# Optimization experiments

Measured on AMD Instinct MI355X. Metric: run time of the kernel, lower is better.

## Reference

```python
import jax, jax.numpy as jnp
import numpy as np

B, C, T, W, H = 2, 256, 16, 64, 64


def setup_inputs():
    key = jax.random.key(0)
    ks = jax.random.split(key, 6)
    C2 = C // 2
    return {
        "x": jax.random.normal(ks[0], (B, C, T, W, H), jnp.float32),
        "Wq": jax.random.normal(ks[1], (3, C2, C), jnp.float32) * 0.02,
        "bq": jnp.zeros((3, C2), jnp.float32),
        "Wk": jax.random.normal(ks[2], (3, C2, C), jnp.float32) * 0.02,
        "bk": jnp.zeros((3, C2), jnp.float32),
        "Wv": jax.random.normal(ks[3], (3, C, C), jnp.float32) * 0.02,
        "bv": jnp.zeros((3, C), jnp.float32),
        "gamma": jax.random.normal(ks[4], (3,), jnp.float32) * 0.1,
    }


def _conv1x1(t, Wm, b):
    # Conv3d with kernel_size=1 == per-voxel channel matmul
    return jnp.einsum('bcijk,oc->boijk', t, Wm) + b[None, :, None, None, None]


def _pool(t):
    # MaxPool3d(kernel=(2,1,1), stride=(2,1,1)) along dim 2 (even length)
    return jnp.maximum(t[:, :, 0::2], t[:, :, 1::2])


def _cell(x, Wq, bq, Wk, bk, Wv, bv, gamma, attn_id):
    Bb, Cc, Tt, Ww, Hh = x.shape
    if attn_id == 'T':
        out = x
    elif attn_id == 'W':
        out = jnp.swapaxes(x, 2, 3)  # [B,C,W,T,H]
    else:
        out = jnp.swapaxes(x, 2, 4)  # [B,C,H,W,T]
    A = out.shape[2]
    # NOTE: these are raw row-major reshapes, faithful to torch .view
    q = _conv1x1(out, Wq, bq).reshape(Bb, A, -1)              # [B, A, C/2*d1*d2]
    k = _pool(_conv1x1(out, Wk, bk)).reshape(Bb, -1, A // 2)  # [B, C/2*d1*d2, A/2]
    attn = jax.nn.softmax(jnp.einsum('bij,bjk->bik', q, k), axis=-1)  # [B, A, A/2]
    v = _pool(_conv1x1(out, Wv, bv)).reshape(Bb, -1, A // 2)  # [B, C*d1*d2, A/2]
    o = jnp.einsum('bxp,bap->bxa', v, attn)                   # [B, X, A]
    if attn_id == 'T':
        o = o.reshape(Bb, Cc, Ww, Hh, Tt).transpose(0, 1, 4, 2, 3)
    elif attn_id == 'W':
        o = o.reshape(Bb, Cc, Tt, Hh, Ww).transpose(0, 1, 2, 4, 3)
    else:
        o = o.reshape(Bb, Cc, Tt, Ww, Hh)
    return gamma * o + x


def reference(x, Wq, bq, Wk, bk, Wv, bv, gamma):
    out = x
    for i, aid in enumerate(('T', 'W', 'H')):
        out = _cell(out, Wq[i], bq[i], Wk[i], bk[i], Wv[i], bv[i], gamma[i], aid)
    return out
```

## Files before the change

### kernel.cpp

```cpp
#include <hip/hip_runtime.h>


constexpr int XBS = 16777216;

typedef __attribute__((ext_vector_type(8)))  short short8v;
typedef __attribute__((ext_vector_type(16))) float f32x16;

__device__ __forceinline__ unsigned rne16(float f) {
    unsigned u = __float_as_uint(f);
    return (u + 0x7FFFu + ((u >> 16) & 1u)) >> 16;
}

__global__ __launch_bounds__(64) void prep_w(
    const float* __restrict__ W, unsigned int* __restrict__ dst)
{
    const int l = threadIdx.x;
    const int ks = blockIdx.x, mf = blockIdx.y, hl = blockIdx.z;
    const float* src = W + (mf * 32 + (l & 31)) * 256 + ks * 16 + ((l >> 5) << 3);
    unsigned pk[4];
    #pragma unroll
    for (int e = 0; e < 4; ++e) {
        float f0 = src[2 * e], f1 = src[2 * e + 1];
        unsigned b0, b1;
        if (hl == 0) {
            b0 = __float_as_uint(f0) >> 16;
            b1 = __float_as_uint(f1) >> 16;
        } else {
            unsigned h0 = __float_as_uint(f0) & 0xFFFF0000u;
            unsigned h1 = __float_as_uint(f1) & 0xFFFF0000u;
            b0 = rne16(f0 - __uint_as_float(h0));
            b1 = rne16(f1 - __uint_as_float(h1));
        }
        pk[e] = b0 | (b1 << 16);
    }
    size_t off = ((size_t)(mf * 16 + ks) * 2 + hl) * 256 + l * 4;
    *(uint4*)&dst[off] = make_uint4(pk[0], pk[1], pk[2], pk[3]);
}

template<int CELL>
__global__ __launch_bounds__(256) void xsplit_kernel(
    const float* __restrict__ src, unsigned int* __restrict__ xTp)
{
    __shared__ float T[64][66];
    const int tid = threadIdx.x;
    const int b = blockIdx.z, cb = blockIdx.y, nb = blockIdx.x;
    const int runbase = (CELL == 0) ? nb * 64
                                    : ((nb & 15) * 4096 + ((nb >> 4) << 6));
    const float* sp = src + (size_t)b * XBS + (size_t)(cb * 64) * 65536 + runbase;
    #pragma unroll
    for (int i = 0; i < 4; ++i) {
        int id = tid + i * 256;
        int cl = id >> 4, rc = (id & 15) * 4;
        const float4 v = *(const float4*)&sp[(size_t)cl * 65536 + rc];
        *(float2*)&T[cl][rc]     = make_float2(v.x, v.y);
        *(float2*)&T[cl][rc + 2] = make_float2(v.z, v.w);
    }
    __syncthreads();
    unsigned int* dst = xTp + (size_t)b * (65536u * 256u);
    #pragma unroll
    for (int ps = 0; ps < 4; ++ps) {
        int r = ps * 16 + (tid >> 4);
        int c0 = (tid & 15) * 4;
        unsigned pk[4];
        #pragma unroll
        for (int e = 0; e < 4; ++e) {
            float f = T[c0 + e][r];
            unsigned hi = __float_as_uint(f) & 0xFFFF0000u;
            pk[e] = hi | rne16(f - __uint_as_float(hi));
        }
        int n_row = (CELL == 2) ? (r * 1024 + nb) : (nb * 64 + r);
        *(uint4*)&dst[(size_t)n_row * 256 + cb * 64 + c0] =
            make_uint4(pk[0], pk[1], pk[2], pk[3]);
    }
}

template<bool POOL, int LGS>
__global__ __launch_bounds__(256, 2) void mconv(
    const unsigned int* __restrict__ xTp, const unsigned int* __restrict__ wf,
    const float* __restrict__ bias, float* __restrict__ out, int obs)
{
    constexpr int NS = POOL ? 32768 : 65536;
    constexpr int MF = POOL ? 2 : 4;
    constexpr int NV = POOL ? 2 : 1;

    __shared__ __align__(16) unsigned short Bh[128 * 64];
    __shared__ __align__(16) unsigned short Bl[128 * 64];

    const int tid = threadIdx.x;
    const int lane = tid & 63, wv = tid >> 6;
    const int b = blockIdx.z, gy = blockIdx.y, nb = blockIdx.x;
    const unsigned int* xb = xTp + (size_t)b * (65536u * 256u);

    f32x16 acc[MF][NV];
    #pragma unroll
    for (int m = 0; m < MF; ++m)
        #pragma unroll
        for (int v = 0; v < NV; ++v)
            #pragma unroll
            for (int r = 0; r < 16; ++r) acc[m][v][r] = 0.f;

    for (int ko = 0; ko < 4; ++ko) {
        const int c0u = ko * 64;
        #pragma unroll
        for (int i = 0; i < 8; ++i) {
            int id = tid + i * 256;
            int row = id >> 4, q4 = id & 15;
            int n_src;
            if (!POOL) n_src = nb * 128 + row;
            else {
                int v = row >> 6, m = nb * 64 + (row & 63);
                int p = m >> LGS, s = m & ((1 << LGS) - 1);
                n_src = ((2 * p + v) << LGS) + s;
            }
            const uint4 g = *(const uint4*)&xb[(size_t)n_src * 256 + c0u + q4 * 4];
            unsigned h01 = (g.x >> 16)     | (g.y & 0xFFFF0000u);
            unsigned h23 = (g.z >> 16)     | (g.w & 0xFFFF0000u);
            unsigned l01 = (g.x & 0xFFFFu) | (g.y << 16);
            unsigned l23 = (g.z & 0xFFFFu) | (g.w << 16);
            int byt = row * 128 + (((q4 >> 1) ^ (row & 7)) << 4) + ((q4 & 1) << 3);
            *(uint2*)((char*)Bh + byt) = make_uint2(h01, h23);
            *(uint2*)((char*)Bl + byt) = make_uint2(l01, l23);
        }
        __syncthreads();
        #pragma unroll
        for (int ks = 0; ks < 4; ++ks) {
            short8v ah[MF], al[MF];
            #pragma unroll
            for (int m = 0; m < MF; ++m) {
                int mfG = gy * 4 + (POOL ? ((wv >> 1) * 2 + m) : m);
                const unsigned int* ap =
                    wf + (size_t)((mfG * 16 + ko * 4 + ks) * 2) * 256 + lane * 4;
                ah[m] = *(const short8v*)ap;
                al[m] = *(const short8v*)(ap + 256);
            }
            #pragma unroll
            for (int v = 0; v < NV; ++v) {
                int row = POOL ? (v * 64 + (wv & 1) * 32 + (lane & 31))
                               : (wv * 32 + (lane & 31));
                int byt = row * 128 + (((ks * 2 + (lane >> 5)) ^ (row & 7)) << 4);
                short8v bh = *(const short8v*)((char*)Bh + byt);
                short8v bl = *(const short8v*)((char*)Bl + byt);
                #pragma unroll
                for (int m = 0; m < MF; ++m) {
                    acc[m][v] = __builtin_amdgcn_mfma_f32_32x32x16_bf16(ah[m], bh, acc[m][v], 0, 0, 0);
                    acc[m][v] = __builtin_amdgcn_mfma_f32_32x32x16_bf16(ah[m], bl, acc[m][v], 0, 0, 0);
                    acc[m][v] = __builtin_amdgcn_mfma_f32_32x32x16_bf16(al[m], bh, acc[m][v], 0, 0, 0);
                }
            }
        }
        __syncthreads();
    }

    float* ob = out + (size_t)b * obs;
    const int colbase = POOL ? (nb * 64 + (wv & 1) * 32 + (lane & 31))
                             : (nb * 128 + wv * 32 + (lane & 31));
    #pragma unroll
    for (int m = 0; m < MF; ++m) {
        int mfG = gy * 4 + (POOL ? ((wv >> 1) * 2 + m) : m);
        #pragma unroll
        for (int r = 0; r < 16; ++r) {
            int o = mfG * 32 + (r & 3) + 8 * (r >> 2) + 4 * (lane >> 5);
            float val = POOL ? fmaxf(acc[m][0][r], acc[m][1][r]) : acc[m][0][r];
            ob[(size_t)o * NS + colbase] = val + bias[o];
        }
    }
}

template<int LGS>
__global__ __launch_bounds__(256, 2) void mconv_v(
    const unsigned int* __restrict__ xTp, const unsigned int* __restrict__ wf,
    const float* __restrict__ bias, float* __restrict__ out)
{
    __shared__ __align__(16) unsigned short Bh[64 * 64];
    __shared__ __align__(16) unsigned short Bl[64 * 64];

    const int tid = threadIdx.x;
    const int lane = tid & 63, wv = tid >> 6;
    const int b = blockIdx.z, nb = blockIdx.x;
    const unsigned int* xb = xTp + (size_t)b * (65536u * 256u);

    f32x16 acc[2][2];
    #pragma unroll
    for (int m = 0; m < 2; ++m)
        #pragma unroll
        for (int v = 0; v < 2; ++v)
            #pragma unroll
            for (int r = 0; r < 16; ++r) acc[m][v][r] = 0.f;

    for (int ko = 0; ko < 4; ++ko) {
        const int c0u = ko * 64;
        #pragma unroll
        for (int i = 0; i < 4; ++i) {
            int id = tid + i * 256;
            int row = id >> 4, q4 = id & 15;
            int v = row >> 5, m = nb * 32 + (row & 31);
            int p = m >> LGS, s = m & ((1 << LGS) - 1);
            int n_src = ((2 * p + v) << LGS) + s;
            const uint4 g = *(const uint4*)&xb[(size_t)n_src * 256 + c0u + q4 * 4];
            unsigned h01 = (g.x >> 16)     | (g.y & 0xFFFF0000u);
            unsigned h23 = (g.z >> 16)     | (g.w & 0xFFFF0000u);
            unsigned l01 = (g.x & 0xFFFFu) | (g.y << 16);
            unsigned l23 = (g.z & 0xFFFFu) | (g.w << 16);
            int byt = row * 128 + (((q4 >> 1) ^ (row & 7)) << 4) + ((q4 & 1) << 3);
            *(uint2*)((char*)Bh + byt) = make_uint2(h01, h23);
            *(uint2*)((char*)Bl + byt) = make_uint2(l01, l23);
        }
        __syncthreads();
        #pragma unroll
        for (int ks = 0; ks < 4; ++ks) {
            short8v ah[2], al[2];
            #pragma unroll
            for (int m = 0; m < 2; ++m) {
                int mfG = wv * 2 + m;
                const unsigned int* ap =
                    wf + (size_t)((mfG * 16 + ko * 4 + ks) * 2) * 256 + lane * 4;
                ah[m] = *(const short8v*)ap;
                al[m] = *(const short8v*)(ap + 256);
            }
            #pragma unroll
            for (int v = 0; v < 2; ++v) {
                int row = v * 32 + (lane & 31);
                int byt = row * 128 + (((ks * 2 + (lane >> 5)) ^ (row & 7)) << 4);
                short8v bh = *(const short8v*)((char*)Bh + byt);
                short8v bl = *(const short8v*)((char*)Bl + byt);
                #pragma unroll
                for (int m = 0; m < 2; ++m) {
                    acc[m][v] = __builtin_amdgcn_mfma_f32_32x32x16_bf16(ah[m], bh, acc[m][v], 0, 0, 0);
                    acc[m][v] = __builtin_amdgcn_mfma_f32_32x32x16_bf16(ah[m], bl, acc[m][v], 0, 0, 0);
                    acc[m][v] = __builtin_amdgcn_mfma_f32_32x32x16_bf16(al[m], bh, acc[m][v], 0, 0, 0);
                }
            }
        }
        __syncthreads();
    }

    float* ob = out + (size_t)b * 8388608;
    const int colbase = nb * 32 + (lane & 31);
    #pragma unroll
    for (int m = 0; m < 2; ++m) {
        int mfG = wv * 2 + m;
        #pragma unroll
        for (int r = 0; r < 16; ++r) {
            int o = mfG * 32 + (r & 3) + 8 * (r >> 2) + 4 * (lane >> 5);
            float val = fmaxf(acc[m][0][r], acc[m][1][r]);
            ob[(size_t)o * 32768 + colbase] = val + bias[o];
        }
    }
}

template<int A, int AH, int PP, int G, int KS, int M>
__global__ __launch_bounds__(256) void logits_kernel(
    const float* __restrict__ qb, const float* __restrict__ kb,
    float* __restrict__ Lpart)
{
    const int tid = threadIdx.x;
    const int jl = tid & 63, pg = tid >> 6;
    const int p0 = pg * PP;
    const int b = blockIdx.z, a0 = blockIdx.y * G, kc = blockIdx.x;
    constexpr int CH = M / KS;
    const float* q = qb + (size_t)b * 8388608 + (size_t)a0 * M + (size_t)kc * CH;
    const float* k = kb + (size_t)b * 4194304;

    float acc[G][PP];
    #pragma unroll
    for (int g = 0; g < G; ++g)
        #pragma unroll
        for (int pp = 0; pp < PP; ++pp) acc[g][pp] = 0.f;

    for (int it = 0; it < CH / 64; ++it) {
        const int jo = jl + it * 64;
        const int j  = kc * CH + jo;
        float qv[G];
        #pragma unroll
        for (int g = 0; g < G; ++g) qv[g] = q[g * M + jo];
        float kv[PP];
        if (PP == 8) {
            float4 k0 = *(const float4*)&k[(size_t)j * AH + p0];
            float4 k1 = *(const float4*)&k[(size_t)j * AH + p0 + 4];
            kv[0]=k0.x; kv[1]=k0.y; kv[2]=k0.z; kv[3]=k0.w;
            kv[4]=k1.x; kv[5]=k1.y; kv[6]=k1.z; kv[7]=k1.w;
        } else {
            float2 k0 = *(const float2*)&k[(size_t)j * AH + p0];
            kv[0]=k0.x; if (PP > 1) kv[1]=k0.y;
        }
        #pragma unroll
        for (int g = 0; g < G; ++g)
            #pragma unroll
            for (int pp = 0; pp < PP; ++pp) acc[g][pp] += qv[g] * kv[pp];
    }

    #pragma unroll
    for (int g = 0; g < G; ++g)
        #pragma unroll
        for (int pp = 0; pp < PP; ++pp) {
            float v = acc[g][pp];
            #pragma unroll
            for (int off = 32; off; off >>= 1) v += __shfl_down(v, off, 64);
            if (jl == 0)
                Lpart[(size_t)(((b * A + a0 + g) * AH) + p0 + pp) * KS + kc] = v;
        }
}

__global__ __launch_bounds__(64) void softmax_kernel(
    const float* __restrict__ Lpart, float* __restrict__ attn,
    int AH, int KS)
{
    const int row = blockIdx.x;
    const int p = threadIdx.x;
    float s = 0.f;
    if (p < AH) {
        const size_t base = (size_t)(row * AH + p) * KS;
        for (int kc = 0; kc < KS; ++kc) s += Lpart[base + kc];
    }
    float m = (p < AH) ? s : -3.4e38f;
    #pragma unroll
    for (int off = 32; off; off >>= 1) m = fmaxf(m, __shfl_xor(m, off, 64));
    float e = (p < AH) ? __expf(s - m) : 0.f;
    float t = e;
    #pragma unroll
    for (int off = 32; off; off >>= 1) t += __shfl_xor(t, off, 64);
    if (p < AH) attn[(size_t)row * AH + p] = e / t;
}

template<int CELL>
__global__ __launch_bounds__(256) void apply_kernel(
    const float* __restrict__ vbuf, const float* __restrict__ attn,
    const float* __restrict__ xsrc, float* __restrict__ xdst,
    const float* __restrict__ gp, int gidx)
{
    constexpr int A  = (CELL == 0) ? 16 : 64;
    constexpr int AH = A / 2;
    constexpr int PADA = AH + 4;
    constexpr int ITERS = (CELL == 1) ? 4 : 2;

    __shared__ float attnA[A * PADA];
    __shared__ float vls[(CELL == 0) ? 4 : 64 * 32];

    const int tid = threadIdx.x;
    const int b = blockIdx.z, c = blockIdx.y;

    for (int idx = tid; idx < A * AH / 4; idx += 256) {
        int a = idx / (AH / 4), q = idx % (AH / 4);
        *(float4*)&attnA[a * PADA + q * 4] =
            *(const float4*)&attn[(size_t)b * A * AH + a * AH + q * 4];
    }

    const float g = gp[gidx];
    const float* xs = xsrc + (size_t)b * XBS + (size_t)c * 65536;
    float*       xd = xdst + (size_t)b * XBS + (size_t)c * 65536;
    const float* vb = vbuf + (size_t)b * 8388608;

    if (CELL == 0) {
        __syncthreads();
        const int i0 = blockIdx.x * 8;
        const int r0 = (tid & 63) * 4;
        const int il = r0 >> 6, j0 = r0 & 63;
        const int a0 = (tid >> 6) * 4;
        float4 aa[2][4];
        #pragma unroll
        for (int ch = 0; ch < 2; ++ch)
            #pragma unroll
            for (int at = 0; at < 4; ++at)
                aa[ch][at] = *(const float4*)&attnA[(a0 + at) * PADA + ch * 4];
        for (int ig = 0; ig < 2; ++ig) {
            const int i = i0 + ig * 4 + il;
            const float* vrow = vb + ((size_t)(c * 64 + i) * 64 + j0) * 8;
            float acc[4][4];
            #pragma unroll
            for (int rt = 0; rt < 4; ++rt)
                #pragma unroll
                for (int at = 0; at < 4; ++at) acc[rt][at] = 0.f;
            #pragma unroll
            for (int ch = 0; ch < 2; ++ch)
                #pragma unroll
                for (int rt = 0; rt < 4; ++rt) {
                    float4 vv = *(const float4*)&vrow[rt * 8 + ch * 4];
                    #pragma unroll
                    for (int at = 0; at < 4; ++at)
                        acc[rt][at] += vv.x * aa[ch][at].x + vv.y * aa[ch][at].y
                                     + vv.z * aa[ch][at].z + vv.w * aa[ch][at].w;
                }
            #pragma unroll
            for (int at = 0; at < 4; ++at) {
                int a = a0 + at;
                size_t xi = (size_t)a * 4096 + i * 64 + j0;
                float4 sv = *(const float4*)&xs[xi];
                *(float4*)&xd[xi] = make_float4(
                    g * acc[0][at] + sv.x, g * acc[1][at] + sv.y,
                    g * acc[2][at] + sv.z, g * acc[3][at] + sv.w);
            }
        }
    } else {
        const int k = tid & 15, r0 = k * 4;
        const int a0 = (tid >> 4) * 4;
        for (int itn = 0; itn < ITERS; ++itn) {
            const int ib = (CELL == 1) ? (blockIdx.x * 4 + itn)
                                       : ((blockIdx.x * 2 + itn) * 4);
            __syncthreads();
            {
                const int rowbase = c * 1024 + ib * ((CELL == 1) ? 64 : 16);
                const float* src = vb + (size_t)rowbase * 32;
                int rr = tid >> 3, cc = tid & 7;
                #pragma unroll
                for (int u = 0; u < 2; ++u) {
                    int r = rr + u * 32;
                    int slot = cc ^ ((r >> 2) & 7);
                    *(float4*)&vls[r * 32 + slot * 4] =
                        *(const float4*)&src[r * 32 + cc * 4];
                }
            }
            __syncthreads();
            float acc[4][4];
            #pragma unroll
            for (int rt = 0; rt < 4; ++rt)
                #pragma unroll
                for (int at = 0; at < 4; ++at) acc[rt][at] = 0.f;
            #pragma unroll
            for (int ch = 0; ch < 8; ++ch) {
                const int slot = (ch ^ (k & 7)) * 4;
                float4 aa[4];
                #pragma unroll
                for (int at = 0; at < 4; ++at)
                    aa[at] = *(const float4*)&attnA[(a0 + at) * PADA + ch * 4];
                #pragma unroll
                for (int rt = 0; rt < 4; ++rt) {
                    float4 vv = *(const float4*)&vls[(r0 + rt) * 32 + slot];
                    #pragma unroll
                    for (int at = 0; at < 4; ++at)
                        acc[rt][at] += vv.x * aa[at].x + vv.y * aa[at].y
                                     + vv.z * aa[at].z + vv.w * aa[at].w;
                }
            }
            if (CELL == 1) {
                const int i = ib, j0 = r0;
                #pragma unroll
                for (int at = 0; at < 4; ++at) {
                    int a = a0 + at;
                    size_t xi = (size_t)i * 4096 + a * 64 + j0;
                    float4 sv = *(const float4*)&xs[xi];
                    *(float4*)&xd[xi] = make_float4(
                        g * acc[0][at] + sv.x, g * acc[1][at] + sv.y,
                        g * acc[2][at] + sv.z, g * acc[3][at] + sv.w);
                }
            } else {
                #pragma unroll
                for (int rt = 0; rt < 4; ++rt) {
                    int r = r0 + rt;
                    int i = ib + (r >> 4), j = r & 15;
                    size_t xi = (size_t)i * 1024 + j * 64 + a0;
                    float4 sv = *(const float4*)&xs[xi];
                    *(float4*)&xd[xi] = make_float4(
                        g * acc[rt][0] + sv.x, g * acc[rt][1] + sv.y,
                        g * acc[rt][2] + sv.z, g * acc[rt][3] + sv.w);
                }
            }
        }
    }
}

extern "C" void kernel_launch(void* const* d_in, const int* in_sizes, int n_in,
                              void* d_out, int out_size, void* d_ws, size_t ws_size,
                              hipStream_t stream)
{
    const float* x  = (const float*)d_in[0];
    const float* Wq = (const float*)d_in[1];
    const float* bq = (const float*)d_in[2];
    const float* Wk = (const float*)d_in[3];
    const float* bk = (const float*)d_in[4];
    const float* Wv = (const float*)d_in[5];
    const float* bv = (const float*)d_in[6];
    const float* gm = (const float*)d_in[7];
    float* out = (float*)d_out;

    float* ws   = (float*)d_ws;
    float* qbuf = ws;
    float* kbuf = qbuf + 16777216;
    float* vbuf = kbuf + 8388608;
    float* Lp   = vbuf + 16777216;
    float* attn = Lp + 65536;
    unsigned int* wfb = (unsigned int*)(attn + 4096);
    unsigned int* xTp = wfb + 3 * 131072;

    dim3 B256(256), B64(64);

    for (int c = 0; c < 3; ++c) {
        unsigned int* wfc = wfb + c * 131072;
        prep_w<<<dim3(16,4,2),B64,0,stream>>>(Wq + c*32768, wfc);
        prep_w<<<dim3(16,4,2),B64,0,stream>>>(Wk + c*32768, wfc + 32768);
        prep_w<<<dim3(16,8,2),B64,0,stream>>>(Wv + c*65536, wfc + 65536);
    }

    xsplit_kernel<0><<<dim3(1024,4,2),B256,0,stream>>>(x, xTp);
    mconv<false,12><<<dim3(512,1,2),B256,0,stream>>>(xTp, wfb,          bq, qbuf, 8388608);
    mconv<true ,12><<<dim3(512,1,2),B256,0,stream>>>(xTp, wfb + 32768,  bk, kbuf, 4194304);
    mconv_v<12><<<dim3(1024,1,2),B256,0,stream>>>(xTp, wfb + 65536,  bv, vbuf);
    logits_kernel<16,8,2,8,128,524288><<<dim3(128,2,2),B256,0,stream>>>(qbuf, kbuf, Lp);
    softmax_kernel<<<dim3(32),B64,0,stream>>>(Lp, attn, 8, 128);
    apply_kernel<0><<<dim3(8,256,2),B256,0,stream>>>(vbuf, attn, x, out, gm, 0);

    unsigned int* wf1 = wfb + 131072;
    xsplit_kernel<1><<<dim3(1024,4,2),B256,0,stream>>>(out, xTp);
    mconv<false,10><<<dim3(512,1,2),B256,0,stream>>>(xTp, wf1,          bq+128, qbuf, 8388608);
    mconv<true ,10><<<dim3(512,1,2),B256,0,stream>>>(xTp, wf1 + 32768,  bk+128, kbuf, 4194304);
    mconv_v<10><<<dim3(1024,1,2),B256,0,stream>>>(xTp, wf1 + 65536,  bv+256, vbuf);
    logits_kernel<64,32,8,8,16,131072><<<dim3(16,8,2),B256,0,stream>>>(qbuf, kbuf, Lp);
    softmax_kernel<<<dim3(128),B64,0,stream>>>(Lp, attn, 32, 16);
    apply_kernel<1><<<dim3(4,256,2),B256,0,stream>>>(vbuf, attn, out, out, gm, 1);

    unsigned int* wf2 = wfb + 262144;
    xsplit_kernel<2><<<dim3(1024,4,2),B256,0,stream>>>(out, xTp);
    mconv<false,10><<<dim3(512,1,2),B256,0,stream>>>(xTp, wf2,          bq+256, qbuf, 8388608);
    mconv<true ,10><<<dim3(512,1,2),B256,0,stream>>>(xTp, wf2 + 32768,  bk+256, kbuf, 4194304);
    mconv_v<10><<<dim3(1024,1,2),B256,0,stream>>>(xTp, wf2 + 65536,  bv+512, vbuf);
    logits_kernel<64,32,8,8,16,131072><<<dim3(16,8,2),B256,0,stream>>>(qbuf, kbuf, Lp);
    softmax_kernel<<<dim3(128),B64,0,stream>>>(Lp, attn, 32, 16);
    apply_kernel<2><<<dim3(8,256,2),B256,0,stream>>>(vbuf, attn, out, out, gm, 2);
}
```

Baseline: 1.231 ms.

## Fuse fp32 input transpose and bf16 split into conv kernels for cells T and W

Adds fconv/fconv_v kernels that read the fp32 activation directly with the cell's strided layout, split each value into bf16 hi/lo parts in registers and stage them into swizzled shared memory. They replace the separate xsplit pass plus mconv for the first two cells. This drops a full write and reread of the split activation buffer, but the input is now read and converted three times (q, k, v) instead of once. Cell H still uses the old path.

```diff
diff --git a/kernel.cpp b/kernel.cpp
--- a/kernel.cpp
+++ b/kernel.cpp
@@ -71,6 +71,219 @@
         int n_row = (CELL == 2) ? (r * 1024 + nb) : (nb * 64 + r);
         *(uint4*)&dst[(size_t)n_row * 256 + cb * 64 + c0] =
             make_uint4(pk[0], pk[1], pk[2], pk[3]);
+    }
+}
+
+template<int CELL, bool POOL>
+__global__ __launch_bounds__(256, 2) void fconv(
+    const float* __restrict__ xf, const unsigned int* __restrict__ wf,
+    const float* __restrict__ bias, float* __restrict__ out, int obs)
+{
+    constexpr int NS = POOL ? 32768 : 65536;
+    constexpr int MF = POOL ? 2 : 4;
+    constexpr int NV = POOL ? 2 : 1;
+
+    __shared__ __align__(16) unsigned short Bh[128 * 64];
+    __shared__ __align__(16) unsigned short Bl[128 * 64];
+
+    const int tid = threadIdx.x;
+    const int lane = tid & 63, wv = tid >> 6;
+    const int b = blockIdx.z, gy = blockIdx.y, nb = blockIdx.x;
+    const float* xb = xf + (size_t)b * XBS;
+
+    f32x16 acc[MF][NV];
+    #pragma unroll
+    for (int m = 0; m < MF; ++m)
+        #pragma unroll
+        for (int v = 0; v < NV; ++v)
+            #pragma unroll
+            for (int r = 0; r < 16; ++r) acc[m][v][r] = 0.f;
+
+    for (int ko = 0; ko < 4; ++ko) {
+        const int c0 = ko * 64;
+        #pragma unroll
+        for (int s = 0; s < 2; ++s) {
+            const int sb = tid + s * 256;
+            const int rq = (sb & 7) | (((sb >> 5) & 3) << 3);
+            const int cq = ((sb >> 3) & 3) | (((sb >> 7) & 3) << 2);
+            const int r4 = rq * 4;
+            int off;
+            if (!POOL) {
+                int n = nb * 128 + r4;
+                off = (CELL == 0) ? n
+                    : ((n >> 6) & 15) * 4096 + ((n >> 10) << 6) + (n & 63);
+            } else {
+                int v = rq >> 4;
+                int m = nb * 64 + (rq & 15) * 4;
+                if (CELL == 0) off = ((2 * (m >> 12) + v) << 12) + (m & 4095);
+                else off = (((m & 1023) >> 6) << 12) + ((2 * (m >> 10) + v) << 6) + (m & 63);
+            }
+            const float* src = xb + (size_t)(c0 + cq * 4) * 65536 + off;
+            float4 f0 = *(const float4*)(src);
+            float4 f1 = *(const float4*)(src + 65536);
+            float4 f2 = *(const float4*)(src + 131072);
+            float4 f3 = *(const float4*)(src + 196608);
+            const float fr[4][4] = {{f0.x,f1.x,f2.x,f3.x},{f0.y,f1.y,f2.y,f3.y},
+                                    {f0.z,f1.z,f2.z,f3.z},{f0.w,f1.w,f2.w,f3.w}};
+            #pragma unroll
+            for (int rn = 0; rn < 4; ++rn) {
+                unsigned h[4], l[4];
+                #pragma unroll
+                for (int e = 0; e < 4; ++e) {
+                    unsigned hi = __float_as_uint(fr[rn][e]) & 0xFFFF0000u;
+                    h[e] = hi;
+                    l[e] = rne16(fr[rn][e] - __uint_as_float(hi));
+                }
+                int row = r4 + rn;
+                int byt = row * 128 + (((cq >> 1) ^ (row & 7)) << 4) + ((cq & 1) << 3);
+                *(uint2*)((char*)Bh + byt) = make_uint2((h[0] >> 16) | h[1],
+                                                        (h[2] >> 16) | h[3]);
+                *(uint2*)((char*)Bl + byt) = make_uint2(l[0] | (l[1] << 16),
+                                                        l[2] | (l[3] << 16));
+            }
+        }
+        __syncthreads();
+        #pragma unroll
+        for (int ks = 0; ks < 4; ++ks) {
+            short8v ah[MF], al[MF];
+            #pragma unroll
+            for (int m = 0; m < MF; ++m) {
+                int mfG = gy * 4 + (POOL ? ((wv >> 1) * 2 + m) : m);
+                const unsigned int* ap =
+                    wf + (size_t)((mfG * 16 + ko * 4 + ks) * 2) * 256 + lane * 4;
+                ah[m] = *(const short8v*)ap;
+                al[m] = *(const short8v*)(ap + 256);
+            }
+            #pragma unroll
+            for (int v = 0; v < NV; ++v) {
+                int row = POOL ? (v * 64 + (wv & 1) * 32 + (lane & 31))
+                               : (wv * 32 + (lane & 31));
+                int byt = row * 128 + (((ks * 2 + (lane >> 5)) ^ (row & 7)) << 4);
+                short8v bh = *(const short8v*)((char*)Bh + byt);
+                short8v bl = *(const short8v*)((char*)Bl + byt);
+                #pragma unroll
+                for (int m = 0; m < MF; ++m) {
+                    acc[m][v] = __builtin_amdgcn_mfma_f32_32x32x16_bf16(ah[m], bh, acc[m][v], 0, 0, 0);
+                    acc[m][v] = __builtin_amdgcn_mfma_f32_32x32x16_bf16(ah[m], bl, acc[m][v], 0, 0, 0);
+                    acc[m][v] = __builtin_amdgcn_mfma_f32_32x32x16_bf16(al[m], bh, acc[m][v], 0, 0, 0);
+                }
+            }
+        }
+        __syncthreads();
+    }
+
+    float* ob = out + (size_t)b * obs;
+    const int colbase = POOL ? (nb * 64 + (wv & 1) * 32 + (lane & 31))
+                             : (nb * 128 + wv * 32 + (lane & 31));
+    #pragma unroll
+    for (int m = 0; m < MF; ++m) {
+        int mfG = gy * 4 + (POOL ? ((wv >> 1) * 2 + m) : m);
+        #pragma unroll
+        for (int r = 0; r < 16; ++r) {
+            int o = mfG * 32 + (r & 3) + 8 * (r >> 2) + 4 * (lane >> 5);
+            float val = POOL ? fmaxf(acc[m][0][r], acc[m][1][r]) : acc[m][0][r];
+            ob[(size_t)o * NS + colbase] = val + bias[o];
+        }
+    }
+}
+
+template<int CELL>
+__global__ __launch_bounds__(256, 2) void fconv_v(
+    const float* __restrict__ xf, const unsigned int* __restrict__ wf,
+    const float* __restrict__ bias, float* __restrict__ out)
+{
+    __shared__ __align__(16) unsigned short Bh[64 * 64];
+    __shared__ __align__(16) unsigned short Bl[64 * 64];
+
+    const int tid = threadIdx.x;
+    const int lane = tid & 63, wv = tid >> 6;
+    const int b = blockIdx.z, nb = blockIdx.x;
+    const float* xb = xf + (size_t)b * XBS;
+
+    f32x16 acc[2][2];
+    #pragma unroll
+    for (int m = 0; m < 2; ++m)
+        #pragma unroll
+        for (int v = 0; v < 2; ++v)
+            #pragma unroll
+            for (int r = 0; r < 16; ++r) acc[m][v][r] = 0.f;
+
+    for (int ko = 0; ko < 4; ++ko) {
+        const int c0 = ko * 64;
+        {
+            const int sb = tid;
+            const int rq = (sb & 7) | (((sb >> 5) & 1) << 3);
+            const int cq = ((sb >> 3) & 3) | (((sb >> 6) & 3) << 2);
+            const int r4 = rq * 4;
+            const int v = rq >> 3;
+            const int m = nb * 32 + (rq & 7) * 4;
+            int off;
+            if (CELL == 0) off = ((2 * (m >> 12) + v) << 12) + (m & 4095);
+            else off = (((m & 1023) >> 6) << 12) + ((2 * (m >> 10) + v) << 6) + (m & 63);
+            const float* src = xb + (size_t)(c0 + cq * 4) * 65536 + off;
+            float4 f0 = *(const float4*)(src);
+            float4 f1 = *(const float4*)(src + 65536);
+            float4 f2 = *(const float4*)(src + 131072);
+            float4 f3 = *(const float4*)(src + 196608);
+            const float fr[4][4] = {{f0.x,f1.x,f2.x,f3.x},{f0.y,f1.y,f2.y,f3.y},
+                                    {f0.z,f1.z,f2.z,f3.z},{f0.w,f1.w,f2.w,f3.w}};
+            #pragma unroll
+            for (int rn = 0; rn < 4; ++rn) {
+                unsigned h[4], l[4];
+                #pragma unroll
+                for (int e = 0; e < 4; ++e) {
+                    unsigned hi = __float_as_uint(fr[rn][e]) & 0xFFFF0000u;
+                    h[e] = hi;
+                    l[e] = rne16(fr[rn][e] - __uint_as_float(hi));
+                }
+                int row = r4 + rn;
+                int byt = row * 128 + (((cq >> 1) ^ (row & 7)) << 4) + ((cq & 1) << 3);
+                *(uint2*)((char*)Bh + byt) = make_uint2((h[0] >> 16) | h[1],
+                                                        (h[2] >> 16) | h[3]);
+                *(uint2*)((char*)Bl + byt) = make_uint2(l[0] | (l[1] << 16),
+                                                        l[2] | (l[3] << 16));
+            }
+        }
+        __syncthreads();
+        #pragma unroll
+        for (int ks = 0; ks < 4; ++ks) {
+            short8v ah[2], al[2];
+            #pragma unroll
+            for (int m = 0; m < 2; ++m) {
+                int mfG = wv * 2 + m;
+                const unsigned int* ap =
+                    wf + (size_t)((mfG * 16 + ko * 4 + ks) * 2) * 256 + lane * 4;
+                ah[m] = *(const short8v*)ap;
+                al[m] = *(const short8v*)(ap + 256);
+            }
+            #pragma unroll
+            for (int v = 0; v < 2; ++v) {
+                int row = v * 32 + (lane & 31);
+                int byt = row * 128 + (((ks * 2 + (lane >> 5)) ^ (row & 7)) << 4);
+                short8v bh = *(const short8v*)((char*)Bh + byt);
+                short8v bl = *(const short8v*)((char*)Bl + byt);
+                #pragma unroll
+                for (int m = 0; m < 2; ++m) {
+                    acc[m][v] = __builtin_amdgcn_mfma_f32_32x32x16_bf16(ah[m], bh, acc[m][v], 0, 0, 0);
+                    acc[m][v] = __builtin_amdgcn_mfma_f32_32x32x16_bf16(ah[m], bl, acc[m][v], 0, 0, 0);
+                    acc[m][v] = __builtin_amdgcn_mfma_f32_32x32x16_bf16(al[m], bh, acc[m][v], 0, 0, 0);
+                }
+            }
+        }
+        __syncthreads();
+    }
+
+    float* ob = out + (size_t)b * 8388608;
+    const int colbase = nb * 32 + (lane & 31);
+    #pragma unroll
+    for (int m = 0; m < 2; ++m) {
+        int mfG = wv * 2 + m;
+        #pragma unroll
+        for (int r = 0; r < 16; ++r) {
+            int o = mfG * 32 + (r & 3) + 8 * (r >> 2) + 4 * (lane >> 5);
+            float val = fmaxf(acc[m][0][r], acc[m][1][r]);
+            ob[(size_t)o * 32768 + colbase] = val + bias[o];
+        }
     }
 }
 
@@ -490,19 +703,17 @@
         prep_w<<<dim3(16,8,2),B64,0,stream>>>(Wv + c*65536, wfc + 65536);
     }
 
-    xsplit_kernel<0><<<dim3(1024,4,2),B256,0,stream>>>(x, xTp);
-    mconv<false,12><<<dim3(512,1,2),B256,0,stream>>>(xTp, wfb,          bq, qbuf, 8388608);
-    mconv<true ,12><<<dim3(512,1,2),B256,0,stream>>>(xTp, wfb + 32768,  bk, kbuf, 4194304);
-    mconv_v<12><<<dim3(1024,1,2),B256,0,stream>>>(xTp, wfb + 65536,  bv, vbuf);
+    fconv<0,false><<<dim3(512,1,2),B256,0,stream>>>(x, wfb,          bq, qbuf, 8388608);
+    fconv<0,true ><<<dim3(512,1,2),B256,0,stream>>>(x, wfb + 32768,  bk, kbuf, 4194304);
+    fconv_v<0><<<dim3(1024,1,2),B256,0,stream>>>(x, wfb + 65536,  bv, vbuf);
     logits_kernel<16,8,2,8,128,524288><<<dim3(128,2,2),B256,0,stream>>>(qbuf, kbuf, Lp);
     softmax_kernel<<<dim3(32),B64,0,stream>>>(Lp, attn, 8, 128);
     apply_kernel<0><<<dim3(8,256,2),B256,0,stream>>>(vbuf, attn, x, out, gm, 0);
 
     unsigned int* wf1 = wfb + 131072;
-    xsplit_kernel<1><<<dim3(1024,4,2),B256,0,stream>>>(out, xTp);
-    mconv<false,10><<<dim3(512,1,2),B256,0,stream>>>(xTp, wf1,          bq+128, qbuf, 8388608);
-    mconv<true ,10><<<dim3(512,1,2),B256,0,stream>>>(xTp, wf1 + 32768,  bk+128, kbuf, 4194304);
-    mconv_v<10><<<dim3(1024,1,2),B256,0,stream>>>(xTp, wf1 + 65536,  bv+256, vbuf);
+    fconv<1,false><<<dim3(512,1,2),B256,0,stream>>>(out, wf1,          bq+128, qbuf, 8388608);
+    fconv<1,true ><<<dim3(512,1,2),B256,0,stream>>>(out, wf1 + 32768,  bk+128, kbuf, 4194304);
+    fconv_v<1><<<dim3(1024,1,2),B256,0,stream>>>(out, wf1 + 65536,  bv+256, vbuf);
     logits_kernel<64,32,8,8,16,131072><<<dim3(16,8,2),B256,0,stream>>>(qbuf, kbuf, Lp);
     softmax_kernel<<<dim3(128),B64,0,stream>>>(Lp, attn, 32, 16);
     apply_kernel<1><<<dim3(4,256,2),B256,0,stream>>>(vbuf, attn, out, out, gm, 1);
```

Measured after the change: 1.137 ms. 7.6% less time.
